# Kernel optimization log

Hardware: AMD Instinct MI355X
Metric: run time of the kernel (lower is better)

## Reference

```python
import jax, jax.numpy as jnp
import numpy as np

N_NODES = 10000
D_FEAT = 128
N_EDGES = 640000


def setup_inputs() -> dict:
    key = jax.random.key(0)
    k1, k2, k3, k4, k5 = jax.random.split(key, 5)
    feat = jax.random.normal(k1, (N_NODES, D_FEAT), dtype=jnp.float32)
    # fc_pool: Linear(D_FEAT, D_FEAT) as in DGL SAGEConv pool aggregator
    W_pool = jax.random.normal(k2, (D_FEAT, D_FEAT), dtype=jnp.float32) / jnp.sqrt(D_FEAT)
    b_pool = jax.random.normal(k3, (D_FEAT,), dtype=jnp.float32) * 0.01
    edge_src = jax.random.randint(k4, (N_EDGES,), 0, N_NODES, dtype=jnp.int32)
    edge_dst = jax.random.randint(k5, (N_EDGES,), 0, N_NODES, dtype=jnp.int32)
    return {"feat": feat, "W_pool": W_pool, "b_pool": b_pool,
            "edge_src": edge_src, "edge_dst": edge_dst}


def reference(feat, W_pool, b_pool, edge_src, edge_dst):
    # feat_drop is identity (p=0 / eval mode)
    # h = relu(fc_pool(feat_src))  -> [N, D]
    h = jax.nn.relu(feat @ W_pool + b_pool)
    # copy_src + fn.max: per-destination max over incoming edge messages
    msgs = h[edge_src]                                   # [E, D] gather
    neigh = jax.ops.segment_max(msgs, edge_dst, num_segments=N_NODES)
    # zero-in-degree nodes get 0 (DGL convention); since msgs >= 0 post-relu,
    # clamping at 0 only affects empty segments (which are -inf).
    neigh = jnp.maximum(neigh, 0.0)
    # pooling_residual: h_neigh + feat_dst
    return neigh + feat
```

## Files before the change

kernel.cpp:

```cpp
#include <hip/hip_runtime.h>
#include <hip/hip_bf16.h>

#define N_NODES 10000
#define D_FEAT 128
#define N_EDGES 640000
#define NCOPY 8
#define SUBCAP 32

__global__ __launch_bounds__(256) void gemm_relu_kernel(
    const float* __restrict__ feat, const float* __restrict__ W,
    const float* __restrict__ b, unsigned* __restrict__ h_u,
    unsigned* __restrict__ counts) {
  __shared__ float fs[8][D_FEAT];
  const int t = threadIdx.x;
  const int blk = blockIdx.x;
  const int gid = blk * 256 + t;
  if (gid < NCOPY * N_NODES) counts[gid] = 0u;

  const int row0 = blk * 8;
  ((float4*)&fs[0][0])[t] = ((const float4*)(feat + row0 * D_FEAT))[t];
  __syncthreads();

  const int c4 = t & 31;
  const int r  = t >> 5;
  const float4* __restrict__ W4 = (const float4*)W;
  float4 acc = make_float4(0.f, 0.f, 0.f, 0.f);
#pragma unroll 8
  for (int k = 0; k < D_FEAT; ++k) {
    const float f = fs[r][k];
    const float4 w = W4[k * 32 + c4];
    acc.x += f * w.x; acc.y += f * w.y; acc.z += f * w.z; acc.w += f * w.w;
  }
  const float4 bb = ((const float4*)b)[c4];
  float v0 = fmaxf(acc.x + bb.x, 0.f);
  float v1 = fmaxf(acc.y + bb.y, 0.f);
  float v2 = fmaxf(acc.z + bb.z, 0.f);
  float v3 = fmaxf(acc.w + bb.w, 0.f);
  __hip_bfloat162 p0 = __float22bfloat162_rn(make_float2(v0, v1));
  __hip_bfloat162 p1 = __float22bfloat162_rn(make_float2(v2, v3));
  uint2 u;
  u.x = *reinterpret_cast<unsigned*>(&p0);
  u.y = *reinterpret_cast<unsigned*>(&p1);
  ((uint2*)h_u)[(row0 + r) * 32 + c4] = u;
}

__device__ __forceinline__ void scat1(int s, int d, unsigned* __restrict__ cnt,
                                      unsigned c, unsigned* __restrict__ elist) {
  unsigned p = atomicAdd(&cnt[d], 1u);
  if (p < SUBCAP) elist[(((unsigned)d * NCOPY + c) << 5) + p] = (unsigned)s;
}

__global__ __launch_bounds__(256) void scatter_kernel(
    const int4* __restrict__ src4, const int4* __restrict__ dst4,
    unsigned* __restrict__ counts, unsigned* __restrict__ elist) {
  const int tid = blockIdx.x * 256 + threadIdx.x;
  const unsigned c = (unsigned)(blockIdx.x & (NCOPY - 1));
  unsigned* __restrict__ cnt = counts + c * N_NODES;
  const int i0 = tid * 2;
#pragma unroll
  for (int q = 0; q < 2; ++q) {
    const int i = i0 + q;
    if (i < N_EDGES / 4) {
      const int4 s = src4[i];
      const int4 d = dst4[i];
      scat1(s.x, d.x, cnt, c, elist);
      scat1(s.y, d.y, cnt, c, elist);
      scat1(s.z, d.z, cnt, c, elist);
      scat1(s.w, d.w, cnt, c, elist);
    }
  }
}

__device__ __forceinline__ void accum_bf16(unsigned u, float& lo, float& hi) {
  lo = fmaxf(lo, __uint_as_float(u << 16));
  hi = fmaxf(hi, __uint_as_float(u & 0xffff0000u));
}

__global__ __launch_bounds__(128) void aggregate_kernel(
    const uint4* __restrict__ h16, const float4* __restrict__ feat4,
    const unsigned* __restrict__ counts, const unsigned* __restrict__ elist,
    float4* __restrict__ out4) {
  const int d = blockIdx.x;
  const int t = threadIdx.x;
  const int slot8 = t >> 4;
  const int j = t & 15;

  __shared__ unsigned sl[NCOPY * SUBCAP];
  __shared__ unsigned nsh[NCOPY];
  __shared__ float red[16][8];

  if (t < NCOPY) nsh[t] = min(counts[t * N_NODES + d], (unsigned)SUBCAP);
  __syncthreads();

  unsigned base[NCOPY];
  unsigned tot = 0;
#pragma unroll
  for (int c = 0; c < NCOPY; ++c) { base[c] = tot; tot += nsh[c]; }

  const unsigned ebeg = (unsigned)d * (NCOPY * SUBCAP);
#pragma unroll
  for (int s = t; s < NCOPY * SUBCAP; s += 128) {
    const unsigned c = (unsigned)s >> 5, p = (unsigned)s & 31u;
    if (p < nsh[c]) sl[base[c] + p] = elist[ebeg + (unsigned)s];
  }
  __syncthreads();

  float m0 = 0.f, m1 = 0.f, m2 = 0.f, m3 = 0.f,
        m4 = 0.f, m5 = 0.f, m6 = 0.f, m7 = 0.f;
  unsigned bpos = 0;
  for (; bpos + 16 <= tot; bpos += 16) {
    const unsigned sA = sl[bpos + slot8];
    const unsigned sB = sl[bpos + 8 + slot8];
    const uint4 qA = h16[sA * 16 + j];
    const uint4 qB = h16[sB * 16 + j];
    accum_bf16(qA.x, m0, m1); accum_bf16(qA.y, m2, m3);
    accum_bf16(qA.z, m4, m5); accum_bf16(qA.w, m6, m7);
    accum_bf16(qB.x, m0, m1); accum_bf16(qB.y, m2, m3);
    accum_bf16(qB.z, m4, m5); accum_bf16(qB.w, m6, m7);
  }
  for (; bpos < tot; bpos += 8) {
    if (bpos + slot8 < tot) {
      const uint4 q = h16[sl[bpos + slot8] * 16 + j];
      accum_bf16(q.x, m0, m1); accum_bf16(q.y, m2, m3);
      accum_bf16(q.z, m4, m5); accum_bf16(q.w, m6, m7);
    }
  }

  m0 = fmaxf(m0, __shfl_xor(m0, 16)); m1 = fmaxf(m1, __shfl_xor(m1, 16));
  m2 = fmaxf(m2, __shfl_xor(m2, 16)); m3 = fmaxf(m3, __shfl_xor(m3, 16));
  m4 = fmaxf(m4, __shfl_xor(m4, 16)); m5 = fmaxf(m5, __shfl_xor(m5, 16));
  m6 = fmaxf(m6, __shfl_xor(m6, 16)); m7 = fmaxf(m7, __shfl_xor(m7, 16));
  m0 = fmaxf(m0, __shfl_xor(m0, 32)); m1 = fmaxf(m1, __shfl_xor(m1, 32));
  m2 = fmaxf(m2, __shfl_xor(m2, 32)); m3 = fmaxf(m3, __shfl_xor(m3, 32));
  m4 = fmaxf(m4, __shfl_xor(m4, 32)); m5 = fmaxf(m5, __shfl_xor(m5, 32));
  m6 = fmaxf(m6, __shfl_xor(m6, 32)); m7 = fmaxf(m7, __shfl_xor(m7, 32));

  if (t >= 64 && t < 80) {
    red[t - 64][0] = m0; red[t - 64][1] = m1; red[t - 64][2] = m2; red[t - 64][3] = m3;
    red[t - 64][4] = m4; red[t - 64][5] = m5; red[t - 64][6] = m6; red[t - 64][7] = m7;
  }
  __syncthreads();
  if (t < 16) {
    m0 = fmaxf(m0, red[t][0]); m1 = fmaxf(m1, red[t][1]);
    m2 = fmaxf(m2, red[t][2]); m3 = fmaxf(m3, red[t][3]);
    m4 = fmaxf(m4, red[t][4]); m5 = fmaxf(m5, red[t][5]);
    m6 = fmaxf(m6, red[t][6]); m7 = fmaxf(m7, red[t][7]);
    const float4 fA = feat4[d * 32 + t * 2];
    const float4 fB = feat4[d * 32 + t * 2 + 1];
    out4[d * 32 + t * 2]     = make_float4(m0 + fA.x, m1 + fA.y, m2 + fA.z, m3 + fA.w);
    out4[d * 32 + t * 2 + 1] = make_float4(m4 + fB.x, m5 + fB.y, m6 + fB.z, m7 + fB.w);
  }
}

extern "C" void kernel_launch(void* const* d_in, const int* in_sizes, int n_in,
                              void* d_out, int out_size, void* d_ws, size_t ws_size,
                              hipStream_t stream) {
  const float* feat   = (const float*)d_in[0];
  const float* W_pool = (const float*)d_in[1];
  const float* b_pool = (const float*)d_in[2];
  const int* edge_src = (const int*)d_in[3];
  const int* edge_dst = (const int*)d_in[4];
  float* out = (float*)d_out;

  char* ws = (char*)d_ws;
  unsigned* h_u    = (unsigned*)(ws);
  unsigned* counts = (unsigned*)(ws + 2560000);
  unsigned* elist  = (unsigned*)(ws + 2880064);

  gemm_relu_kernel<<<N_NODES / 8, 256, 0, stream>>>(feat, W_pool, b_pool, h_u, counts);
  const int nthr = N_EDGES / 8;
  scatter_kernel<<<(nthr + 255) / 256, 256, 0, stream>>>(
      (const int4*)edge_src, (const int4*)edge_dst, counts, elist);
  aggregate_kernel<<<N_NODES, 128, 0, stream>>>(
      (const uint4*)h_u, (const float4*)feat, counts, elist, (float4*)out);
}
```

Baseline: 133.6 us.

## Replace global-atomic edge bucketing with per-block LDS histogram, column scan, scatter

Replaces the scatter that used global atomics into 8 sub-copy counters with a two-pass counting sort. 128 blocks each build an LDS histogram of destinations, a column scan turns these into per-block offsets, and a second pass scatters sources into a single 128-slot list per node using LDS atomics. This removes global atomic contention and simplifies the aggregate kernel's list compaction. The cost is two extra launches and a 5 MB histogram buffer that is written and read twice, plus only 128 blocks in the hist and scatter passes.

```diff
diff --git a/kernel.cpp b/kernel.cpp
--- a/kernel.cpp
+++ b/kernel.cpp
@@ -4,20 +4,16 @@
 #define N_NODES 10000
 #define D_FEAT 128
 #define N_EDGES 640000
-#define NCOPY 8
-#define SUBCAP 32
+#define NB 128
+#define EPB 5000
+#define CAP 128
 
 __global__ __launch_bounds__(256) void gemm_relu_kernel(
     const float* __restrict__ feat, const float* __restrict__ W,
-    const float* __restrict__ b, unsigned* __restrict__ h_u,
-    unsigned* __restrict__ counts) {
+    const float* __restrict__ b, unsigned* __restrict__ h_u) {
   __shared__ float fs[8][D_FEAT];
   const int t = threadIdx.x;
-  const int blk = blockIdx.x;
-  const int gid = blk * 256 + t;
-  if (gid < NCOPY * N_NODES) counts[gid] = 0u;
-
-  const int row0 = blk * 8;
+  const int row0 = blockIdx.x * 8;
   ((float4*)&fs[0][0])[t] = ((const float4*)(feat + row0 * D_FEAT))[t];
   __syncthreads();
 
@@ -44,29 +40,64 @@
   ((uint2*)h_u)[(row0 + r) * 32 + c4] = u;
 }
 
-__device__ __forceinline__ void scat1(int s, int d, unsigned* __restrict__ cnt,
-                                      unsigned c, unsigned* __restrict__ elist) {
-  unsigned p = atomicAdd(&cnt[d], 1u);
-  if (p < SUBCAP) elist[(((unsigned)d * NCOPY + c) << 5) + p] = (unsigned)s;
+__global__ __launch_bounds__(256) void hist_kernel(
+    const int4* __restrict__ dst4, unsigned* __restrict__ bh) {
+  __shared__ unsigned cnt[N_NODES];
+  const int t = threadIdx.x;
+  const int b = blockIdx.x;
+  for (int i = t; i < N_NODES; i += 256) cnt[i] = 0u;
+  __syncthreads();
+  const int base4 = b * (EPB / 4);
+#pragma unroll
+  for (int q = 0; q < 5; ++q) {
+    const int i = q * 256 + t;
+    if (i < EPB / 4) {
+      const int4 d = dst4[base4 + i];
+      atomicAdd(&cnt[d.x], 1u); atomicAdd(&cnt[d.y], 1u);
+      atomicAdd(&cnt[d.z], 1u); atomicAdd(&cnt[d.w], 1u);
+    }
+  }
+  __syncthreads();
+  unsigned* __restrict__ row = bh + (size_t)b * N_NODES;
+  for (int i = t; i < N_NODES; i += 256) row[i] = cnt[i];
+}
+
+__global__ __launch_bounds__(256) void colscan_kernel(
+    unsigned* __restrict__ bh, unsigned* __restrict__ cnt_total) {
+  const int d = blockIdx.x * 256 + threadIdx.x;
+  if (d >= N_NODES) return;
+  unsigned run = 0;
+#pragma unroll 8
+  for (int b = 0; b < NB; ++b) {
+    const size_t idx = (size_t)b * N_NODES + d;
+    const unsigned v = bh[idx];
+    bh[idx] = run;
+    run += v;
+  }
+  cnt_total[d] = run;
 }
 
 __global__ __launch_bounds__(256) void scatter_kernel(
     const int4* __restrict__ src4, const int4* __restrict__ dst4,
-    unsigned* __restrict__ counts, unsigned* __restrict__ elist) {
-  const int tid = blockIdx.x * 256 + threadIdx.x;
-  const unsigned c = (unsigned)(blockIdx.x & (NCOPY - 1));
-  unsigned* __restrict__ cnt = counts + c * N_NODES;
-  const int i0 = tid * 2;
+    const unsigned* __restrict__ bh, unsigned* __restrict__ elist) {
+  __shared__ unsigned cnt[N_NODES];
+  const int t = threadIdx.x;
+  const int b = blockIdx.x;
+  for (int i = t; i < N_NODES; i += 256) cnt[i] = 0u;
+  __syncthreads();
+  const unsigned* __restrict__ row = bh + (size_t)b * N_NODES;
+  const int base4 = b * (EPB / 4);
 #pragma unroll
-  for (int q = 0; q < 2; ++q) {
-    const int i = i0 + q;
-    if (i < N_EDGES / 4) {
-      const int4 s = src4[i];
-      const int4 d = dst4[i];
-      scat1(s.x, d.x, cnt, c, elist);
-      scat1(s.y, d.y, cnt, c, elist);
-      scat1(s.z, d.z, cnt, c, elist);
-      scat1(s.w, d.w, cnt, c, elist);
+  for (int q = 0; q < 5; ++q) {
+    const int i = q * 256 + t;
+    if (i < EPB / 4) {
+      const int4 s = src4[base4 + i];
+      const int4 d = dst4[base4 + i];
+      unsigned p;
+      p = atomicAdd(&cnt[d.x], 1u) + row[d.x]; if (p < CAP) elist[((unsigned)d.x << 7) + p] = (unsigned)s.x;
+      p = atomicAdd(&cnt[d.y], 1u) + row[d.y]; if (p < CAP) elist[((unsigned)d.y << 7) + p] = (unsigned)s.y;
+      p = atomicAdd(&cnt[d.z], 1u) + row[d.z]; if (p < CAP) elist[((unsigned)d.z << 7) + p] = (unsigned)s.z;
+      p = atomicAdd(&cnt[d.w], 1u) + row[d.w]; if (p < CAP) elist[((unsigned)d.w << 7) + p] = (unsigned)s.w;
     }
   }
 }
@@ -78,37 +109,24 @@
 
 __global__ __launch_bounds__(128) void aggregate_kernel(
     const uint4* __restrict__ h16, const float4* __restrict__ feat4,
-    const unsigned* __restrict__ counts, const unsigned* __restrict__ elist,
+    const unsigned* __restrict__ cnt_total, const unsigned* __restrict__ elist,
     float4* __restrict__ out4) {
   const int d = blockIdx.x;
   const int t = threadIdx.x;
   const int slot8 = t >> 4;
   const int j = t & 15;
 
-  __shared__ unsigned sl[NCOPY * SUBCAP];
-  __shared__ unsigned nsh[NCOPY];
+  __shared__ unsigned sl[CAP];
   __shared__ float red[16][8];
 
-  if (t < NCOPY) nsh[t] = min(counts[t * N_NODES + d], (unsigned)SUBCAP);
-  __syncthreads();
-
-  unsigned base[NCOPY];
-  unsigned tot = 0;
-#pragma unroll
-  for (int c = 0; c < NCOPY; ++c) { base[c] = tot; tot += nsh[c]; }
-
-  const unsigned ebeg = (unsigned)d * (NCOPY * SUBCAP);
-#pragma unroll
-  for (int s = t; s < NCOPY * SUBCAP; s += 128) {
-    const unsigned c = (unsigned)s >> 5, p = (unsigned)s & 31u;
-    if (p < nsh[c]) sl[base[c] + p] = elist[ebeg + (unsigned)s];
-  }
+  const unsigned n = min(cnt_total[d], (unsigned)CAP);
+  if ((unsigned)t < n) sl[t] = elist[((unsigned)d << 7) + (unsigned)t];
   __syncthreads();
 
   float m0 = 0.f, m1 = 0.f, m2 = 0.f, m3 = 0.f,
         m4 = 0.f, m5 = 0.f, m6 = 0.f, m7 = 0.f;
   unsigned bpos = 0;
-  for (; bpos + 16 <= tot; bpos += 16) {
+  for (; bpos + 16 <= n; bpos += 16) {
     const unsigned sA = sl[bpos + slot8];
     const unsigned sB = sl[bpos + 8 + slot8];
     const uint4 qA = h16[sA * 16 + j];
@@ -118,8 +136,8 @@
     accum_bf16(qB.x, m0, m1); accum_bf16(qB.y, m2, m3);
     accum_bf16(qB.z, m4, m5); accum_bf16(qB.w, m6, m7);
   }
-  for (; bpos < tot; bpos += 8) {
-    if (bpos + slot8 < tot) {
+  for (; bpos < n; bpos += 8) {
+    if (bpos + slot8 < n) {
       const uint4 q = h16[sl[bpos + slot8] * 16 + j];
       accum_bf16(q.x, m0, m1); accum_bf16(q.y, m2, m3);
       accum_bf16(q.z, m4, m5); accum_bf16(q.w, m6, m7);
@@ -163,14 +181,16 @@
   float* out = (float*)d_out;
 
   char* ws = (char*)d_ws;
-  unsigned* h_u    = (unsigned*)(ws);
-  unsigned* counts = (unsigned*)(ws + 2560000);
-  unsigned* elist  = (unsigned*)(ws + 2880064);
+  unsigned* h_u       = (unsigned*)(ws);
+  unsigned* bh        = (unsigned*)(ws + 2560000);
+  unsigned* cnt_total = (unsigned*)(ws + 7680000);
+  unsigned* elist     = (unsigned*)(ws + 7720064);
 
-  gemm_relu_kernel<<<N_NODES / 8, 256, 0, stream>>>(feat, W_pool, b_pool, h_u, counts);
-  const int nthr = N_EDGES / 8;
-  scatter_kernel<<<(nthr + 255) / 256, 256, 0, stream>>>(
-      (const int4*)edge_src, (const int4*)edge_dst, counts, elist);
+  gemm_relu_kernel<<<N_NODES / 8, 256, 0, stream>>>(feat, W_pool, b_pool, h_u);
+  hist_kernel<<<NB, 256, 0, stream>>>((const int4*)edge_dst, bh);
+  colscan_kernel<<<(N_NODES + 255) / 256, 256, 0, stream>>>(bh, cnt_total);
+  scatter_kernel<<<NB, 256, 0, stream>>>(
+      (const int4*)edge_src, (const int4*)edge_dst, bh, elist);
   aggregate_kernel<<<N_NODES, 128, 0, stream>>>(
-      (const uint4*)h_u, (const float4*)feat, counts, elist, (float4*)out);
+      (const uint4*)h_u, (const float4*)feat, cnt_total, elist, (float4*)out);
 }
```

Measured after the change: 128.0 us. 4.2% less time.
